# Kernel optimization log

Hardware: AMD Instinct MI355X
Metric: run time of the kernel (lower is better)

## Reference

```python
import jax, jax.numpy as jnp
import numpy as np

NEG_SLOPE = 0.01  # torch F.leaky_relu default


def setup_inputs() -> dict:
    key = jax.random.key(0)
    k1, k2, k3, k4, k5 = jax.random.split(key, 5)
    n_nodes, d_node = 50000, 128
    n_edges = 600000
    in_feat, out_feat = 2 * d_node, 128
    return {
        "n_f": jax.random.normal(k1, (n_nodes, d_node), dtype=jnp.float32),
        "W_edge": jax.random.normal(k2, (out_feat, in_feat), dtype=jnp.float32) * (1.0 / np.sqrt(in_feat)),
        "W_attn": jax.random.normal(k3, (1, out_feat), dtype=jnp.float32) * (1.0 / np.sqrt(out_feat)),
        "src_idx": jax.random.randint(k4, (n_edges,), 0, n_nodes, dtype=jnp.int64),
        "dst_idx": jax.random.randint(k5, (n_edges,), 0, n_nodes, dtype=jnp.int64),
    }


def reference(n_f, W_edge, W_attn, src_idx, dst_idx):
    # Gather per-edge src/dst node features and concat: [E, 2*d]
    feat = jnp.concatenate([n_f[src_idx], n_f[dst_idx]], axis=1)
    # edge_fn (no bias) + sigmoid activation: [E, out_feat]
    e_feat = jax.nn.sigmoid(jnp.einsum("ei,oi->eo", feat, W_edge))
    # attn_fc (no bias): [E, 1]
    a_feat = jnp.einsum("eo,ao->ea", e_feat, W_attn)
    a_fact = jnp.where(a_feat >= 0, a_feat, NEG_SLOPE * a_feat)
    # softmax over dim=1 (size 1 -> all ones, kept faithful to the original)
    alpha = jax.nn.softmax(a_fact, axis=1)
    return e_feat, alpha
```

## Files before the change

kernel.cpp:

```cpp
#include <hip/hip_runtime.h>
#include <hip/hip_bf16.h>

#define N_NODES  50000
#define D_NODE   128
#define E_TOTAL  600000
#define IN_FEAT  256
#define OUT_FEAT 128
#define ALPHA_OFF (600000 * 128)

typedef __bf16 bf16x8 __attribute__((ext_vector_type(8)));
typedef __bf16 bf16x4 __attribute__((ext_vector_type(4)));
typedef float  f32x4  __attribute__((ext_vector_type(4)));


__global__ void convert_wcat(const float* __restrict__ W, __bf16* __restrict__ wl) {
    int gid  = blockIdx.x * 256 + threadIdx.x;
    int lane = gid & 63;
    int nk   = gid >> 6;
    int n    = nk & 15;
    int kk   = nk >> 4;
    int o2   = n * 16 + (lane & 15);
    int k2   = kk * 32 + (lane >> 4) * 8;
    const float* src = (o2 < 128) ? (W + o2 * IN_FEAT + k2)
                                  : (W + (o2 - 128) * IN_FEAT + 128 + k2);
    bf16x8 h;
    #pragma unroll
    for (int j = 0; j < 8; ++j) h[j] = (__bf16)src[j];
    *(bf16x8*)(wl + gid * 8) = h;
}

__launch_bounds__(64)
__global__ void zgemm(const float* __restrict__ n_f,
                      const __bf16* __restrict__ wl,
                      __bf16* __restrict__ Z) {
    const int lane = threadIdx.x;
    const int v0   = blockIdx.x * 16;
    const int lr   = lane & 15;
    const int lg   = lane >> 4;

    f32x4 acc[16];
    #pragma unroll
    for (int n = 0; n < 16; ++n) acc[n] = (f32x4){0.f, 0.f, 0.f, 0.f};

    #pragma unroll
    for (int kk = 0; kk < 4; ++kk) {
        const float* ap = n_f + (v0 + lr) * D_NODE + kk * 32 + lg * 8;
        float4 v0f = *(const float4*)ap;
        float4 v1f = *(const float4*)(ap + 4);
        bf16x8 a;
        a[0] = (__bf16)v0f.x; a[1] = (__bf16)v0f.y;
        a[2] = (__bf16)v0f.z; a[3] = (__bf16)v0f.w;
        a[4] = (__bf16)v1f.x; a[5] = (__bf16)v1f.y;
        a[6] = (__bf16)v1f.z; a[7] = (__bf16)v1f.w;
        const bf16x8* bp = (const bf16x8*)(wl) + kk * 16 * 64 + lane;
        #pragma unroll
        for (int n = 0; n < 16; ++n) {
            bf16x8 b = bp[n * 64];
            acc[n] = __builtin_amdgcn_mfma_f32_16x16x32_bf16(a, b, acc[n], 0, 0, 0);
        }
    }

    #pragma unroll
    for (int n = 0; n < 16; ++n) {
        const int col = n * 16 + lr;
        #pragma unroll
        for (int j = 0; j < 4; ++j)
            Z[(v0 + lg * 4 + j) * 256 + col] = (__bf16)acc[n][j];
    }
}

__launch_bounds__(256)
__global__ void edge_apply(const __bf16* __restrict__ Z,
                           const int* __restrict__ src_idx,
                           const int* __restrict__ dst_idx,
                           float* __restrict__ out) {
    const int t  = blockIdx.x * 256 + threadIdx.x;
    const int e  = t >> 5;
    const int c4 = (t & 31) * 4;

    const int sv = src_idx[e];
    const int dv = dst_idx[e];

    if ((t & 31) == 0) out[ALPHA_OFF + e] = 1.0f;

    bf16x4 zs = *(const bf16x4*)(Z + sv * 256 + c4);
    bf16x4 zd = *(const bf16x4*)(Z + dv * 256 + 128 + c4);

    f32x4 r;
    #pragma unroll
    for (int j = 0; j < 4; ++j) {
        float x = (float)zs[j] + (float)zd[j];
        r[j] = __builtin_amdgcn_rcpf(1.0f + __expf(-x));
    }
    __builtin_nontemporal_store(r, (f32x4*)(out + e * OUT_FEAT + c4));
}

__global__ void convert_w_fb(const float* __restrict__ W, __bf16* __restrict__ wl) {
    int gid = blockIdx.x * 256 + threadIdx.x;
    int lane = gid & 63;
    int nk   = gid >> 6;
    int n    = nk & 7;
    int kk   = nk >> 3;
    int row  = n * 16 + (lane & 15);
    int col  = kk * 32 + (lane >> 4) * 8;
    const float* src = W + row * IN_FEAT + col;
    bf16x8 h;
    #pragma unroll
    for (int j = 0; j < 8; ++j) h[j] = (__bf16)src[j];
    *(bf16x8*)(wl + gid * 8) = h;
}

__launch_bounds__(64, 2)
__global__ void edge_kernel_fb(const float* __restrict__ n_f,
                               const __bf16* __restrict__ wl,
                               const int*   __restrict__ src_idx,
                               const int*   __restrict__ dst_idx,
                               float* __restrict__ out) {
    const int lane = threadIdx.x;
    const int e0   = blockIdx.x * 64;
    const int lr   = lane & 15;
    const int lg   = lane >> 4;

    out[ALPHA_OFF + e0 + lane] = 1.0f;

    int sn[4], dn[4];
    #pragma unroll
    for (int r = 0; r < 4; ++r) {
        const int e = e0 + r * 16 + lr;
        sn[r] = src_idx[e];
        dn[r] = dst_idx[e];
    }
    f32x4 acc[4][8];
    #pragma unroll
    for (int r = 0; r < 4; ++r)
        #pragma unroll
        for (int n = 0; n < 8; ++n) acc[r][n] = (f32x4){0.f, 0.f, 0.f, 0.f};

    #pragma unroll
    for (int kk = 0; kk < 8; ++kk) {
        bf16x8 a[4];
        #pragma unroll
        for (int r = 0; r < 4; ++r) {
            const int node = (kk < 4) ? sn[r] : dn[r];
            const float* ap = n_f + node * D_NODE + (kk & 3) * 32 + lg * 8;
            float4 u0 = *(const float4*)ap;
            float4 u1 = *(const float4*)(ap + 4);
            a[r][0] = (__bf16)u0.x; a[r][1] = (__bf16)u0.y;
            a[r][2] = (__bf16)u0.z; a[r][3] = (__bf16)u0.w;
            a[r][4] = (__bf16)u1.x; a[r][5] = (__bf16)u1.y;
            a[r][6] = (__bf16)u1.z; a[r][7] = (__bf16)u1.w;
        }
        const bf16x8* bp = (const bf16x8*)(wl) + kk * 8 * 64 + lane;
        #pragma unroll
        for (int n = 0; n < 8; ++n) {
            bf16x8 b = bp[n * 64];
            #pragma unroll
            for (int r = 0; r < 4; ++r)
                acc[r][n] = __builtin_amdgcn_mfma_f32_16x16x32_bf16(a[r], b, acc[r][n], 0, 0, 0);
        }
    }
    #pragma unroll
    for (int r = 0; r < 4; ++r) {
        const int ebase = e0 + r * 16 + lg * 4;
        #pragma unroll
        for (int n = 0; n < 8; ++n) {
            const int col = n * 16 + lr;
            #pragma unroll
            for (int j = 0; j < 4; ++j) {
                float x = acc[r][n][j];
                out[(ebase + j) * OUT_FEAT + col] = __builtin_amdgcn_rcpf(1.0f + __expf(-x));
            }
        }
    }
}

extern "C" void kernel_launch(void* const* d_in, const int* in_sizes, int n_in,
                              void* d_out, int out_size, void* d_ws, size_t ws_size,
                              hipStream_t stream) {
    const float* n_f    = (const float*)d_in[0];
    const float* W_edge = (const float*)d_in[1];
    const int* src_idx  = (const int*)d_in[3];
    const int* dst_idx  = (const int*)d_in[4];
    float* out = (float*)d_out;

    const size_t need = 65536 + (size_t)N_NODES * 256 * sizeof(__bf16);
    if (ws_size >= need) {
        __bf16* wl = (__bf16*)d_ws;
        __bf16* Z  = (__bf16*)((char*)d_ws + 65536);
        convert_wcat<<<16, 256, 0, stream>>>(W_edge, wl);
        zgemm<<<N_NODES / 16, 64, 0, stream>>>(n_f, wl, Z);
        edge_apply<<<(E_TOTAL * 32) / 256, 256, 0, stream>>>(Z, src_idx, dst_idx, out);
    } else {
        __bf16* wl = (__bf16*)d_ws;
        convert_w_fb<<<16, 256, 0, stream>>>(W_edge, wl);
        edge_kernel_fb<<<E_TOTAL / 64, 64, 0, stream>>>(n_f, wl, src_idx, dst_idx, out);
    }
}
```

Measured before the change: 109.2 us.

## Bucket edges by source node range so each XCD gathers a localized Z slice

Adds a counting-sort pipeline (histogram, scan, scatter) that groups edges into 64 buckets by source-node range, interleaves the buckets so blocks landing on the same XCD work on neighboring node ranges, and runs the edge apply kernel through this permutation. The aim is better L2 hit rates on the Z gathers for the source side. The cost is four extra kernel launches, atomics, a 2.4MB permutation buffer, one more indirection per edge, and output writes that are no longer in edge order. It also assumes 9750 slots per XCD are enough, which depends on how evenly the random indices spread across buckets.

```diff
diff --git a/kernel.cpp b/kernel.cpp
--- a/kernel.cpp
+++ b/kernel.cpp
@@ -7,10 +7,17 @@
 #define IN_FEAT  256
 #define OUT_FEAT 128
 #define ALPHA_OFF (600000 * 128)
+#define NB       64
+#define HBLK     1024
+#define NHB      586
+#define SLOTS    9750
 
 typedef __bf16 bf16x8 __attribute__((ext_vector_type(8)));
 typedef __bf16 bf16x4 __attribute__((ext_vector_type(4)));
 typedef float  f32x4  __attribute__((ext_vector_type(4)));
+
+__device__ __forceinline__ int bucket_of(int node) { return node / 782; }
+__device__ __forceinline__ int sortbin_of(int b)   { return ((b & 7) << 3) | (b >> 3); }
 
 
 __global__ void convert_wcat(const float* __restrict__ W, __bf16* __restrict__ wl) {
@@ -59,7 +66,6 @@
             acc[n] = __builtin_amdgcn_mfma_f32_16x16x32_bf16(a, b, acc[n], 0, 0, 0);
         }
     }
-
     #pragma unroll
     for (int n = 0; n < 16; ++n) {
         const int col = n * 16 + lr;
@@ -67,6 +73,92 @@
         for (int j = 0; j < 4; ++j)
             Z[(v0 + lg * 4 + j) * 256 + col] = (__bf16)acc[n][j];
     }
+}
+
+__global__ void k_init(int* __restrict__ hist) {
+    if (threadIdx.x < NB) hist[threadIdx.x] = 0;
+}
+
+__global__ void k_hist(const int* __restrict__ src, int* __restrict__ hist) {
+    __shared__ int cnt[NB];
+    const int t = threadIdx.x;
+    if (t < NB) cnt[t] = 0;
+    __syncthreads();
+    const int e = blockIdx.x * HBLK + t;
+    if (e < E_TOTAL) atomicAdd(&cnt[sortbin_of(bucket_of(src[e]))], 1);
+    __syncthreads();
+    if (t < NB && cnt[t] > 0) atomicAdd(&hist[t], cnt[t]);
+}
+
+__global__ void k_scan(const int* __restrict__ hist, int* __restrict__ cursor,
+                       int* __restrict__ xbase) {
+    __shared__ int h[NB];
+    const int t = threadIdx.x;
+    if (t < NB) h[t] = hist[t];
+    __syncthreads();
+    if (t == 0) {
+        int run = 0;
+        for (int sb = 0; sb < NB; ++sb) {
+            if ((sb & 7) == 0) xbase[sb >> 3] = run;
+            cursor[sb] = run;
+            run += h[sb];
+        }
+        xbase[8] = run;
+    }
+}
+
+__global__ void k_scatter(const int* __restrict__ src, int* __restrict__ perm,
+                          int* __restrict__ cursor) {
+    __shared__ int cnt[NB];
+    __shared__ int base[NB];
+    const int t = threadIdx.x;
+    if (t < NB) cnt[t] = 0;
+    __syncthreads();
+    const int e = blockIdx.x * HBLK + t;
+    int sb = 0, lofs = 0;
+    if (e < E_TOTAL) {
+        sb = sortbin_of(bucket_of(src[e]));
+        lofs = atomicAdd(&cnt[sb], 1);
+    }
+    __syncthreads();
+    if (t < NB) base[t] = (cnt[t] > 0) ? atomicAdd(&cursor[t], cnt[t]) : 0;
+    __syncthreads();
+    if (e < E_TOTAL) perm[base[sb] + lofs] = e;
+}
+
+__launch_bounds__(256)
+__global__ void edge_apply_b(const __bf16* __restrict__ Z,
+                             const int* __restrict__ src_idx,
+                             const int* __restrict__ dst_idx,
+                             const int* __restrict__ perm,
+                             const int* __restrict__ xbase,
+                             float* __restrict__ out) {
+    const int j  = blockIdx.x;
+    const int x  = j & 7;
+    const int s  = j >> 3;
+    const int t  = threadIdx.x;
+    const int le = t >> 5;
+    const int c4 = (t & 31) * 4;
+
+    const int pos = xbase[x] + s * 8 + le;
+    if (pos >= xbase[x + 1]) return;
+    const int e  = perm[pos];
+
+    const int sv = src_idx[e];
+    const int dv = dst_idx[e];
+
+    if ((t & 31) == 0) out[ALPHA_OFF + e] = 1.0f;
+
+    bf16x4 zs = *(const bf16x4*)(Z + sv * 256 + c4);
+    bf16x4 zd = *(const bf16x4*)(Z + dv * 256 + 128 + c4);
+
+    f32x4 r;
+    #pragma unroll
+    for (int q = 0; q < 4; ++q) {
+        float xx = (float)zs[q] + (float)zd[q];
+        r[q] = __builtin_amdgcn_rcpf(1.0f + __expf(-xx));
+    }
+    __builtin_nontemporal_store(r, (f32x4*)(out + e * OUT_FEAT + c4));
 }
 
 __launch_bounds__(256)
@@ -77,20 +169,16 @@
     const int t  = blockIdx.x * 256 + threadIdx.x;
     const int e  = t >> 5;
     const int c4 = (t & 31) * 4;
-
     const int sv = src_idx[e];
     const int dv = dst_idx[e];
-
     if ((t & 31) == 0) out[ALPHA_OFF + e] = 1.0f;
-
     bf16x4 zs = *(const bf16x4*)(Z + sv * 256 + c4);
     bf16x4 zd = *(const bf16x4*)(Z + dv * 256 + 128 + c4);
-
     f32x4 r;
     #pragma unroll
-    for (int j = 0; j < 4; ++j) {
-        float x = (float)zs[j] + (float)zd[j];
-        r[j] = __builtin_amdgcn_rcpf(1.0f + __expf(-x));
+    for (int q = 0; q < 4; ++q) {
+        float xx = (float)zs[q] + (float)zd[q];
+        r[q] = __builtin_amdgcn_rcpf(1.0f + __expf(-xx));
     }
     __builtin_nontemporal_store(r, (f32x4*)(out + e * OUT_FEAT + c4));
 }
@@ -167,8 +255,8 @@
             const int col = n * 16 + lr;
             #pragma unroll
             for (int j = 0; j < 4; ++j) {
-                float x = acc[r][n][j];
-                out[(ebase + j) * OUT_FEAT + col] = __builtin_amdgcn_rcpf(1.0f + __expf(-x));
+                float xx = acc[r][n][j];
+                out[(ebase + j) * OUT_FEAT + col] = __builtin_amdgcn_rcpf(1.0f + __expf(-xx));
             }
         }
     }
@@ -183,10 +271,33 @@
     const int* dst_idx  = (const int*)d_in[4];
     float* out = (float*)d_out;
 
-    const size_t need = 65536 + (size_t)N_NODES * 256 * sizeof(__bf16);
-    if (ws_size >= need) {
-        __bf16* wl = (__bf16*)d_ws;
-        __bf16* Z  = (__bf16*)((char*)d_ws + 65536);
+    const size_t off_wl   = 0;
+    const size_t off_Z    = 65536;
+    const size_t off_perm = off_Z + (size_t)N_NODES * 256 * 2;
+    const size_t off_hist = off_perm + (size_t)E_TOTAL * 4;
+    const size_t off_cur  = off_hist + NB * 4;
+    const size_t off_xb   = off_cur + NB * 4;
+    const size_t need_sort  = off_xb + 9 * 4;
+    const size_t need_plain = off_perm;
+
+    if (ws_size >= need_sort) {
+        __bf16* wl   = (__bf16*)((char*)d_ws + off_wl);
+        __bf16* Z    = (__bf16*)((char*)d_ws + off_Z);
+        int* perm    = (int*)((char*)d_ws + off_perm);
+        int* hist    = (int*)((char*)d_ws + off_hist);
+        int* cursor  = (int*)((char*)d_ws + off_cur);
+        int* xbase   = (int*)((char*)d_ws + off_xb);
+
+        convert_wcat<<<16, 256, 0, stream>>>(W_edge, wl);
+        zgemm<<<N_NODES / 16, 64, 0, stream>>>(n_f, wl, Z);
+        k_init<<<1, 128, 0, stream>>>(hist);
+        k_hist<<<NHB, HBLK, 0, stream>>>(src_idx, hist);
+        k_scan<<<1, 64, 0, stream>>>(hist, cursor, xbase);
+        k_scatter<<<NHB, HBLK, 0, stream>>>(src_idx, perm, cursor);
+        edge_apply_b<<<SLOTS * 8, 256, 0, stream>>>(Z, src_idx, dst_idx, perm, xbase, out);
+    } else if (ws_size >= need_plain) {
+        __bf16* wl = (__bf16*)((char*)d_ws + off_wl);
+        __bf16* Z  = (__bf16*)((char*)d_ws + off_Z);
         convert_wcat<<<16, 256, 0, stream>>>(W_edge, wl);
         zgemm<<<N_NODES / 16, 64, 0, stream>>>(n_f, wl, Z);
         edge_apply<<<(E_TOTAL * 32) / 256, 256, 0, stream>>>(Z, src_idx, dst_idx, out);
```

After: 144.9 us. 32.6% more time.
